# Optimization experiments

Measured on AMD Instinct MI355X. Metric: run time of the kernel, lower is better.

Reference implementation:

```python
import jax, jax.numpy as jnp
import numpy as np

N_SLOTS, KEY_DIM, VAL_DIM = 8192, 64, 64
B, S, TOPK = 8, 2048, 8


def setup_inputs() -> dict:
    key = jax.random.key(0)
    k1, k2, k3, k4, k5 = jax.random.split(key, 5)
    queries = jax.random.normal(k1, (B, S, KEY_DIM), dtype=jnp.float32)
    keys_mem = jax.random.normal(k2, (N_SLOTS, KEY_DIM), dtype=jnp.float32) * 0.02
    vals_mem = jax.random.normal(k3, (N_SLOTS, VAL_DIM), dtype=jnp.float32) * 0.02
    fast_vals = jax.random.normal(k4, (N_SLOTS, VAL_DIM), dtype=jnp.float32) * 0.01
    timestamps = jax.random.uniform(k5, (N_SLOTS,), dtype=jnp.float32)
    return {
        "queries": queries,
        "keys_mem": keys_mem,
        "vals_mem": vals_mem,
        "fast_vals": fast_vals,
        "timestamps": timestamps,
        "topk": TOPK,
    }


def reference(queries, keys_mem, vals_mem, fast_vals, timestamps, topk):
    # sim: [B, S, n_slots], scaled dot-product vs. memory keys
    scale = keys_mem.shape[1] ** (-0.5)
    sim = jnp.einsum("bsd,nd->bsn", queries, keys_mem) * scale
    # topk indices computed on detached scores (torch uses sim.detach())
    _, idx = jax.lax.top_k(jax.lax.stop_gradient(sim), topk)  # idx: [B, S, k]
    # gather topk similarities (torch does this via one-hot * sim; same math)
    sim_topk = jnp.take_along_axis(sim, idx, axis=-1)  # [B, S, k]
    # effective memory = slow + fast store; gather rows (torch: one_hot @ memory)
    effective_memory = vals_mem + fast_vals  # [n_slots, val_dim]
    gathered_vals = effective_memory[idx]  # [B, S, k, val_dim]
    attn_weights = jax.nn.softmax(sim_topk, axis=-1)  # [B, S, k]
    weighted_vals = gathered_vals * attn_weights[..., None]  # [B, S, k, val_dim]
    ts_retrieved = timestamps[idx]  # [B, S, k]
    return weighted_vals, idx, ts_retrieved
```

## Files before the change

### kernel.cpp

```cpp
#include <hip/hip_runtime.h>
#include <math.h>

#define NQ      16384
#define NSLOTS  8192
#define D       64
#define K       8

#define WV_ELEMS  (NQ * K * D)
#define IDX_OFF   (WV_ELEMS)
#define TSO_OFF   (IDX_OFF + NQ * K)

#define QPB    32
#define BLOCK  512
#define WAVES  8
#define SPW    (NSLOTS / WAVES)
#define ITERS  (SPW / 32)

using short8  = __attribute__((ext_vector_type(8))) short;
using bf16x8  = __attribute__((ext_vector_type(8))) __bf16;
using f32x4   = __attribute__((ext_vector_type(4))) float;

#define MFMA_BF16(A, B, C) __builtin_amdgcn_mfma_f32_16x16x32_bf16((A), (B), (C), 0, 0, 0)

__device__ __forceinline__ bf16x8 load_frag(const unsigned short* p) {
    short8 s = *reinterpret_cast<const short8*>(p);
    return __builtin_bit_cast(bf16x8, s);
}

__device__ __forceinline__ float packkey(float s, int code) {
    unsigned u = __float_as_uint(s) & 0xFFFFE000u;
    return __uint_as_float(u | (unsigned)code);
}

__device__ __forceinline__ void ins8(float (&tv)[8], float key) {
    float k2 = fmaxf(key, tv[0]);
    float o0 = fminf(tv[1], k2);
    float o1 = __builtin_amdgcn_fmed3f(tv[1], tv[2], k2);
    float o2 = __builtin_amdgcn_fmed3f(tv[2], tv[3], k2);
    float o3 = __builtin_amdgcn_fmed3f(tv[3], tv[4], k2);
    float o4 = __builtin_amdgcn_fmed3f(tv[4], tv[5], k2);
    float o5 = __builtin_amdgcn_fmed3f(tv[5], tv[6], k2);
    float o6 = __builtin_amdgcn_fmed3f(tv[6], tv[7], k2);
    float o7 = fmaxf(tv[7], k2);
    tv[0]=o0; tv[1]=o1; tv[2]=o2; tv[3]=o3; tv[4]=o4; tv[5]=o5; tv[6]=o6; tv[7]=o7;
}

__device__ __forceinline__ void cs(float& a, float& b) {
    const float lo = fminf(a, b), hi = fmaxf(a, b);
    a = lo; b = hi;
}
__device__ __forceinline__ void sort_bitonic8(float (&v)[8]) {
    cs(v[0],v[4]); cs(v[1],v[5]); cs(v[2],v[6]); cs(v[3],v[7]);
    cs(v[0],v[2]); cs(v[1],v[3]); cs(v[4],v[6]); cs(v[5],v[7]);
    cs(v[0],v[1]); cs(v[2],v[3]); cs(v[4],v[5]); cs(v[6],v[7]);
}

__device__ __forceinline__ unsigned short f2bf(float f) {
    unsigned u = __float_as_uint(f);
    return (unsigned short)((u + 0x7FFFu + ((u >> 16) & 1u)) >> 16);
}

__global__ __launch_bounds__(256)
void conv_kernel(const float* __restrict__ q, const float* __restrict__ k,
                 unsigned short* __restrict__ ws) {
    const int t = blockIdx.x * blockDim.x + threadIdx.x;
    if (t < 262144) {
        float4 v = reinterpret_cast<const float4*>(q)[t];
        unsigned long long r =
              (unsigned long long)f2bf(v.x * 0.125f)
            | ((unsigned long long)f2bf(v.y * 0.125f) << 16)
            | ((unsigned long long)f2bf(v.z * 0.125f) << 32)
            | ((unsigned long long)f2bf(v.w * 0.125f) << 48);
        reinterpret_cast<unsigned long long*>(ws + 524288)[t] = r;
    } else if (t < 393216) {
        const int i = t - 262144;
        float4 v = reinterpret_cast<const float4*>(k)[i];
        unsigned long long r =
              (unsigned long long)f2bf(v.x)
            | ((unsigned long long)f2bf(v.y) << 16)
            | ((unsigned long long)f2bf(v.z) << 32)
            | ((unsigned long long)f2bf(v.w) << 48);
        reinterpret_cast<unsigned long long*>(ws)[i] = r;
    }
}

__global__ __launch_bounds__(BLOCK, 4)
void ltm_mfma_kernel(const float* __restrict__ queries,
                     const float* __restrict__ keys_mem,
                     const float* __restrict__ vals_mem,
                     const float* __restrict__ fast_vals,
                     const float* __restrict__ timestamps,
                     const unsigned short* __restrict__ kb,
                     const unsigned short* __restrict__ qb,
                     float* __restrict__ out)
{
    __shared__ float candk[QPB][68];

    const int tid  = threadIdx.x;
    const int lane = tid & 63;
    const int w    = tid >> 6;
    const int row  = lane & 15;
    const int g    = lane >> 4;
    const int g4   = g * 4;
    const int koff = g * 8;
    const int qbase = blockIdx.x * QPB;

    const unsigned short* qpA = qb + (size_t)(qbase + row) * D + koff;
    const bf16x8 bA0 = load_frag(qpA);
    const bf16x8 bA1 = load_frag(qpA + 32);
    const bf16x8 bB0 = load_frag(qpA + 16 * D);
    const bf16x8 bB1 = load_frag(qpA + 16 * D + 32);

    float tvA[8], tvB[8];
    #pragma unroll
    for (int i = 0; i < 8; ++i) { tvA[i] = -INFINITY; tvB[i] = -INFINITY; }

    const int wbase = w * SPW;
    const unsigned short* kp0 = kb + (size_t)(wbase + row) * D + koff;
    bf16x8 a00 = load_frag(kp0);
    bf16x8 a01 = load_frag(kp0 + 32);
    bf16x8 a10 = load_frag(kp0 + 16 * D);
    bf16x8 a11 = load_frag(kp0 + 16 * D + 32);

    int codeA = 8191 - (wbase + g4);

    #pragma unroll 2
    for (int it = 0; it < ITERS; ++it) {
        const int snext = wbase + (it + 1) * 32;
        const unsigned short* np_ = kb + (size_t)(snext + row) * D + koff;
        bf16x8 n00 = load_frag(np_);
        bf16x8 n01 = load_frag(np_ + 32);
        bf16x8 n10 = load_frag(np_ + 16 * D);
        bf16x8 n11 = load_frag(np_ + 16 * D + 32);

        const f32x4 z = {0.f, 0.f, 0.f, 0.f};
        f32x4 c00 = MFMA_BF16(a00, bA0, z);  c00 = MFMA_BF16(a01, bA1, c00);
        f32x4 c01 = MFMA_BF16(a00, bB0, z);  c01 = MFMA_BF16(a01, bB1, c01);
        f32x4 c10 = MFMA_BF16(a10, bA0, z);  c10 = MFMA_BF16(a11, bA1, c10);
        f32x4 c11 = MFMA_BF16(a10, bB0, z);  c11 = MFMA_BF16(a11, bB1, c11);

        ins8(tvA, packkey(c00[0], codeA     ));
        ins8(tvA, packkey(c00[1], codeA -  1));
        ins8(tvA, packkey(c00[2], codeA -  2));
        ins8(tvA, packkey(c00[3], codeA -  3));
        ins8(tvA, packkey(c10[0], codeA - 16));
        ins8(tvA, packkey(c10[1], codeA - 17));
        ins8(tvA, packkey(c10[2], codeA - 18));
        ins8(tvA, packkey(c10[3], codeA - 19));
        ins8(tvB, packkey(c01[0], codeA     ));
        ins8(tvB, packkey(c01[1], codeA -  1));
        ins8(tvB, packkey(c01[2], codeA -  2));
        ins8(tvB, packkey(c01[3], codeA -  3));
        ins8(tvB, packkey(c11[0], codeA - 16));
        ins8(tvB, packkey(c11[1], codeA - 17));
        ins8(tvB, packkey(c11[2], codeA - 18));
        ins8(tvB, packkey(c11[3], codeA - 19));

        codeA -= 32;
        a00 = n00; a01 = n01; a10 = n10; a11 = n11;
    }

    {
        float sA[8], sB[8];
        #pragma unroll
        for (int j = 0; j < 8; ++j) {
            sA[j] = __shfl_xor(tvA[j], 32, 64);
            sB[j] = __shfl_xor(tvB[j], 32, 64);
        }
        float mA[8], mB[8];
        #pragma unroll
        for (int j = 0; j < 8; ++j) {
            mA[j] = fmaxf(tvA[j], sA[7 - j]);
            mB[j] = fmaxf(tvB[j], sB[7 - j]);
        }
        sort_bitonic8(mA);
        sort_bitonic8(mB);
        #pragma unroll
        for (int j = 0; j < 8; ++j) {
            sA[j] = __shfl_xor(mA[j], 16, 64);
            sB[j] = __shfl_xor(mB[j], 16, 64);
        }
        if (g == 0) {
            #pragma unroll
            for (int j = 0; j < 8; ++j) {
                candk[row     ][w * 8 + j] = fmaxf(mA[j], sA[7 - j]);
                candk[row + 16][w * 8 + j] = fmaxf(mB[j], sB[7 - j]);
            }
        }
    }
    __syncthreads();

    const int ql = tid >> 4;
    const int ls = tid & 15;
    const int q  = qbase + ql;

    const float4 qc = reinterpret_cast<const float4*>(queries)[q * 16 + ls];

    unsigned long long tk[8];
    #pragma unroll
    for (int i = 0; i < 8; ++i) tk[i] = 0ull;

    for (int j = 0; j < 64; ++j) {
        const float fk  = candk[ql][j];
        const int   sid = 8191 - (int)(__float_as_uint(fk) & 8191u);
        const float4 kc = reinterpret_cast<const float4*>(keys_mem)[sid * 16 + ls];
        float p = qc.x * kc.x;
        p = fmaf(qc.y, kc.y, p);
        p = fmaf(qc.z, kc.z, p);
        p = fmaf(qc.w, kc.w, p);
        p += __shfl_xor(p, 1, 64);
        p += __shfl_xor(p, 2, 64);
        p += __shfl_xor(p, 4, 64);
        p += __shfl_xor(p, 8, 64);
        const float s = p * 0.125f;
        const unsigned u  = __float_as_uint(s);
        const unsigned ou = (u & 0x80000000u) ? ~u : (u | 0x80000000u);
        const unsigned long long key =
            ((unsigned long long)ou << 13) | (unsigned)(8191 - sid);
        if (key > tk[0]) {
            tk[0] = key;
            #pragma unroll
            for (int uu = 0; uu < 7; ++uu) {
                const bool sw = tk[uu] > tk[uu + 1];
                const unsigned long long x = sw ? tk[uu + 1] : tk[uu];
                const unsigned long long y = sw ? tk[uu]     : tk[uu + 1];
                tk[uu] = x; tk[uu + 1] = y;
            }
        }
    }

    float wv[K]; int wi[K];
    #pragma unroll
    for (int r = 0; r < K; ++r) {
        const unsigned long long best = tk[7 - r];
        const int      sid = 8191 - (int)(best & 8191ull);
        const unsigned ou  = (unsigned)(best >> 13);
        const unsigned ub  = (ou & 0x80000000u) ? (ou & 0x7FFFFFFFu) : ~ou;
        wv[r] = __uint_as_float(ub);
        wi[r] = sid;
    }
    const float m = wv[0];
    float e[K]; float sum = 0.f;
    #pragma unroll
    for (int r = 0; r < K; ++r) { e[r] = expf(wv[r] - m); sum += e[r]; }
    const float inv = 1.f / sum;

    {
        const int   r   = ls >> 1;
        const int   h   = ls & 1;
        const int   id  = wi[r];
        const float wgt = e[r] * inv;
        const float4* vp = reinterpret_cast<const float4*>(vals_mem)  + (size_t)id * 16 + h * 8;
        const float4* fp = reinterpret_cast<const float4*>(fast_vals) + (size_t)id * 16 + h * 8;
        float4* op = reinterpret_cast<float4*>(out + ((size_t)(q * K + r)) * D + h * 32);
        #pragma unroll
        for (int i = 0; i < 8; ++i) {
            const float4 a = vp[i];
            const float4 b = fp[i];
            float4 c;
            c.x = (a.x + b.x) * wgt;
            c.y = (a.y + b.y) * wgt;
            c.z = (a.z + b.z) * wgt;
            c.w = (a.w + b.w) * wgt;
            op[i] = c;
        }
        if (ls < 8) {
            out[IDX_OFF + (size_t)q * K + ls] = (float)wi[ls];
        } else {
            const int r2 = ls - 8;
            out[TSO_OFF + (size_t)q * K + r2] = timestamps[wi[r2]];
        }
    }
}

#define FQPB   32
#define FTPQ   8
#define FBLOCK 256
#define FTS    128
#define FLDK   68
#define FNTILES (NSLOTS / FTS)

__global__ __launch_bounds__(FBLOCK, 2)
void ltm_fused_kernel(const float* __restrict__ queries,
                      const float* __restrict__ keys_mem,
                      const float* __restrict__ vals_mem,
                      const float* __restrict__ fast_vals,
                      const float* __restrict__ timestamps,
                      float* __restrict__ out)
{
    __shared__ float kt[FTS * FLDK];
    __shared__ float candv[FQPB][FTPQ * K];
    __shared__ int   candi[FQPB][FTPQ * K];
    __shared__ float selw[FQPB][K];
    __shared__ int   seli[FQPB][K];

    const int tid = threadIdx.x;
    const int ql  = tid / FTPQ;
    const int sub = tid % FTPQ;
    const int q   = blockIdx.x * FQPB + ql;

    float4 qv[D / 4];
    {
        const float4* qp = reinterpret_cast<const float4*>(queries + (size_t)q * D);
        #pragma unroll
        for (int i = 0; i < D / 4; ++i) qv[i] = qp[i];
    }

    float tv[K]; int ti[K];
    #pragma unroll
    for (int i = 0; i < K; ++i) { tv[i] = -INFINITY; ti[i] = 0; }

    for (int tile = 0; tile < FNTILES; ++tile) {
        __syncthreads();
        {
            const float4* kg = reinterpret_cast<const float4*>(keys_mem + (size_t)tile * FTS * D);
            #pragma unroll
            for (int i = 0; i < (FTS * D / 4) / FBLOCK; ++i) {
                const int e = tid + i * FBLOCK;
                const int row = e >> 4;
                const int col = e & 15;
                *reinterpret_cast<float4*>(&kt[row * FLDK + col * 4]) = kg[e];
            }
        }
        __syncthreads();

        #pragma unroll 4
        for (int j = 0; j < FTS / FTPQ; ++j) {
            const int local = sub + j * FTPQ;
            const float* kr = &kt[local * FLDK];
            float4 a0 = make_float4(0.f, 0.f, 0.f, 0.f);
            float4 a1 = make_float4(0.f, 0.f, 0.f, 0.f);
            #pragma unroll
            for (int i = 0; i < D / 4; i += 2) {
                const float4 k0 = *reinterpret_cast<const float4*>(&kr[(i + 0) * 4]);
                const float4 k1 = *reinterpret_cast<const float4*>(&kr[(i + 1) * 4]);
                a0.x = fmaf(k0.x, qv[i].x, a0.x);   a0.y = fmaf(k0.y, qv[i].y, a0.y);
                a0.z = fmaf(k0.z, qv[i].z, a0.z);   a0.w = fmaf(k0.w, qv[i].w, a0.w);
                a1.x = fmaf(k1.x, qv[i+1].x, a1.x); a1.y = fmaf(k1.y, qv[i+1].y, a1.y);
                a1.z = fmaf(k1.z, qv[i+1].z, a1.z); a1.w = fmaf(k1.w, qv[i+1].w, a1.w);
            }
            float s = ((a0.x + a1.x) + (a0.y + a1.y)) + ((a0.z + a1.z) + (a0.w + a1.w));
            s *= 0.125f;
            const int gid = tile * FTS + local;
            if (s > tv[0]) {
                tv[0] = s; ti[0] = gid;
                #pragma unroll
                for (int u = 0; u < K - 1; ++u) {
                    const bool sw = tv[u] > tv[u + 1];
                    const float va = sw ? tv[u + 1] : tv[u];
                    const float vb = sw ? tv[u]     : tv[u + 1];
                    const int   ia = sw ? ti[u + 1] : ti[u];
                    const int   ib = sw ? ti[u]     : ti[u + 1];
                    tv[u] = va; tv[u + 1] = vb; ti[u] = ia; ti[u + 1] = ib;
                }
            }
        }
    }

    #pragma unroll
    for (int i = 0; i < K; ++i) {
        candv[ql][sub * K + i] = tv[i];
        candi[ql][sub * K + i] = ti[i];
    }
    __syncthreads();

    if (sub == 0) {
        float wv[K]; int wi[K];
        #pragma unroll
        for (int r = 0; r < K; ++r) {
            float bv = -INFINITY; int bi = 0x7fffffff; int bp = 0;
            for (int c = 0; c < FTPQ * K; ++c) {
                const float v = candv[ql][c];
                const int  id = candi[ql][c];
                if ((v > bv) || (v == bv && id < bi)) { bv = v; bi = id; bp = c; }
            }
            candv[ql][bp] = -INFINITY;
            wv[r] = bv; wi[r] = bi;
        }
        const float m = wv[0];
        float e[K]; float sum = 0.f;
        #pragma unroll
        for (int r = 0; r < K; ++r) { e[r] = expf(wv[r] - m); sum += e[r]; }
        const float inv = 1.f / sum;
        #pragma unroll
        for (int r = 0; r < K; ++r) { selw[ql][r] = e[r] * inv; seli[ql][r] = wi[r]; }
    }
    __syncthreads();

    {
        const int r = sub;
        const int id = seli[ql][r];
        const float w = selw[ql][r];
        const float4* vp = reinterpret_cast<const float4*>(vals_mem  + (size_t)id * D);
        const float4* fp = reinterpret_cast<const float4*>(fast_vals + (size_t)id * D);
        float4* op = reinterpret_cast<float4*>(out + (size_t)(q * K + r) * D);
        #pragma unroll
        for (int i = 0; i < D / 4; ++i) {
            const float4 a = vp[i];
            const float4 b = fp[i];
            float4 c;
            c.x = (a.x + b.x) * w; c.y = (a.y + b.y) * w;
            c.z = (a.z + b.z) * w; c.w = (a.w + b.w) * w;
            op[i] = c;
        }
        out[IDX_OFF + (size_t)q * K + r] = (float)id;
        out[TSO_OFF + (size_t)q * K + r] = timestamps[id];
    }
}

extern "C" void kernel_launch(void* const* d_in, const int* in_sizes, int n_in,
                              void* d_out, int out_size, void* d_ws, size_t ws_size,
                              hipStream_t stream) {
    (void)in_sizes; (void)n_in; (void)out_size;
    const float* queries    = (const float*)d_in[0];
    const float* keys_mem   = (const float*)d_in[1];
    const float* vals_mem   = (const float*)d_in[2];
    const float* fast_vals  = (const float*)d_in[3];
    const float* timestamps = (const float*)d_in[4];
    float* out = (float*)d_out;

    if (ws_size >= (size_t)3 * 1024 * 1024) {
        unsigned short* ws = (unsigned short*)d_ws;
        conv_kernel<<<1536, 256, 0, stream>>>(queries, keys_mem, ws);
        ltm_mfma_kernel<<<NQ / QPB, BLOCK, 0, stream>>>(
            queries, keys_mem, vals_mem, fast_vals, timestamps,
            ws , ws + 524288 , out);
    } else {
        ltm_fused_kernel<<<NQ / FQPB, FBLOCK, 0, stream>>>(
            queries, keys_mem, vals_mem, fast_vals, timestamps, out);
    }
}
```

Measured before the change: 126.9 us.

## Halve queries per block to 16 and remap refine/output phase to 32 lanes per query

Cuts queries per block from 32 to 16, so each wave computes only one 16-query MFMA column group and keeps one top-8 list instead of two. Occupancy hints rise to 8 blocks per CU and the grid doubles. The fp32 re-scoring and output phase now uses 32 lanes per query with float2 loads and an extra shuffle step. Per-block register pressure drops, but each key fragment loaded is reused across half as many queries, doubling key traffic and MFMA issue per useful score.

```diff
diff --git a/kernel.cpp b/kernel.cpp
--- a/kernel.cpp
+++ b/kernel.cpp
@@ -10,7 +10,7 @@
 #define IDX_OFF   (WV_ELEMS)
 #define TSO_OFF   (IDX_OFF + NQ * K)
 
-#define QPB    32
+#define QPB    16
 #define BLOCK  512
 #define WAVES  8
 #define SPW    (NSLOTS / WAVES)
@@ -84,7 +84,7 @@
     }
 }
 
-__global__ __launch_bounds__(BLOCK, 4)
+__global__ __launch_bounds__(BLOCK, 8)
 void ltm_mfma_kernel(const float* __restrict__ queries,
                      const float* __restrict__ keys_mem,
                      const float* __restrict__ vals_mem,
@@ -108,12 +108,10 @@
     const unsigned short* qpA = qb + (size_t)(qbase + row) * D + koff;
     const bf16x8 bA0 = load_frag(qpA);
     const bf16x8 bA1 = load_frag(qpA + 32);
-    const bf16x8 bB0 = load_frag(qpA + 16 * D);
-    const bf16x8 bB1 = load_frag(qpA + 16 * D + 32);
-
-    float tvA[8], tvB[8];
-    #pragma unroll
-    for (int i = 0; i < 8; ++i) { tvA[i] = -INFINITY; tvB[i] = -INFINITY; }
+
+    float tvA[8];
+    #pragma unroll
+    for (int i = 0; i < 8; ++i) tvA[i] = -INFINITY;
 
     const int wbase = w * SPW;
     const unsigned short* kp0 = kb + (size_t)(wbase + row) * D + koff;
@@ -134,84 +132,62 @@
         bf16x8 n11 = load_frag(np_ + 16 * D + 32);
 
         const f32x4 z = {0.f, 0.f, 0.f, 0.f};
-        f32x4 c00 = MFMA_BF16(a00, bA0, z);  c00 = MFMA_BF16(a01, bA1, c00);
-        f32x4 c01 = MFMA_BF16(a00, bB0, z);  c01 = MFMA_BF16(a01, bB1, c01);
-        f32x4 c10 = MFMA_BF16(a10, bA0, z);  c10 = MFMA_BF16(a11, bA1, c10);
-        f32x4 c11 = MFMA_BF16(a10, bB0, z);  c11 = MFMA_BF16(a11, bB1, c11);
-
-        ins8(tvA, packkey(c00[0], codeA     ));
-        ins8(tvA, packkey(c00[1], codeA -  1));
-        ins8(tvA, packkey(c00[2], codeA -  2));
-        ins8(tvA, packkey(c00[3], codeA -  3));
-        ins8(tvA, packkey(c10[0], codeA - 16));
-        ins8(tvA, packkey(c10[1], codeA - 17));
-        ins8(tvA, packkey(c10[2], codeA - 18));
-        ins8(tvA, packkey(c10[3], codeA - 19));
-        ins8(tvB, packkey(c01[0], codeA     ));
-        ins8(tvB, packkey(c01[1], codeA -  1));
-        ins8(tvB, packkey(c01[2], codeA -  2));
-        ins8(tvB, packkey(c01[3], codeA -  3));
-        ins8(tvB, packkey(c11[0], codeA - 16));
-        ins8(tvB, packkey(c11[1], codeA - 17));
-        ins8(tvB, packkey(c11[2], codeA - 18));
-        ins8(tvB, packkey(c11[3], codeA - 19));
+        f32x4 c0 = MFMA_BF16(a00, bA0, z);  c0 = MFMA_BF16(a01, bA1, c0);
+        f32x4 c1 = MFMA_BF16(a10, bA0, z);  c1 = MFMA_BF16(a11, bA1, c1);
+
+        ins8(tvA, packkey(c0[0], codeA     ));
+        ins8(tvA, packkey(c0[1], codeA -  1));
+        ins8(tvA, packkey(c0[2], codeA -  2));
+        ins8(tvA, packkey(c0[3], codeA -  3));
+        ins8(tvA, packkey(c1[0], codeA - 16));
+        ins8(tvA, packkey(c1[1], codeA - 17));
+        ins8(tvA, packkey(c1[2], codeA - 18));
+        ins8(tvA, packkey(c1[3], codeA - 19));
 
         codeA -= 32;
         a00 = n00; a01 = n01; a10 = n10; a11 = n11;
     }
 
     {
-        float sA[8], sB[8];
-        #pragma unroll
-        for (int j = 0; j < 8; ++j) {
-            sA[j] = __shfl_xor(tvA[j], 32, 64);
-            sB[j] = __shfl_xor(tvB[j], 32, 64);
-        }
-        float mA[8], mB[8];
-        #pragma unroll
-        for (int j = 0; j < 8; ++j) {
-            mA[j] = fmaxf(tvA[j], sA[7 - j]);
-            mB[j] = fmaxf(tvB[j], sB[7 - j]);
-        }
+        float sA[8];
+        #pragma unroll
+        for (int j = 0; j < 8; ++j) sA[j] = __shfl_xor(tvA[j], 32, 64);
+        float mA[8];
+        #pragma unroll
+        for (int j = 0; j < 8; ++j) mA[j] = fmaxf(tvA[j], sA[7 - j]);
         sort_bitonic8(mA);
-        sort_bitonic8(mB);
-        #pragma unroll
-        for (int j = 0; j < 8; ++j) {
-            sA[j] = __shfl_xor(mA[j], 16, 64);
-            sB[j] = __shfl_xor(mB[j], 16, 64);
-        }
+        #pragma unroll
+        for (int j = 0; j < 8; ++j) sA[j] = __shfl_xor(mA[j], 16, 64);
         if (g == 0) {
             #pragma unroll
-            for (int j = 0; j < 8; ++j) {
-                candk[row     ][w * 8 + j] = fmaxf(mA[j], sA[7 - j]);
-                candk[row + 16][w * 8 + j] = fmaxf(mB[j], sB[7 - j]);
-            }
+            for (int j = 0; j < 8; ++j)
+                candk[row][w * 8 + j] = fmaxf(mA[j], sA[7 - j]);
         }
     }
     __syncthreads();
 
-    const int ql = tid >> 4;
-    const int ls = tid & 15;
-    const int q  = qbase + ql;
-
-    const float4 qc = reinterpret_cast<const float4*>(queries)[q * 16 + ls];
+    const int h  = lane >> 5;
+    const int ls = lane & 31;
+    const int qi = 2 * w + h;
+    const int q  = qbase + qi;
+
+    const float2 qc = reinterpret_cast<const float2*>(queries)[q * 32 + ls];
 
     unsigned long long tk[8];
     #pragma unroll
     for (int i = 0; i < 8; ++i) tk[i] = 0ull;
 
     for (int j = 0; j < 64; ++j) {
-        const float fk  = candk[ql][j];
+        const float fk  = candk[qi][j];
         const int   sid = 8191 - (int)(__float_as_uint(fk) & 8191u);
-        const float4 kc = reinterpret_cast<const float4*>(keys_mem)[sid * 16 + ls];
+        const float2 kc = reinterpret_cast<const float2*>(keys_mem)[sid * 32 + ls];
         float p = qc.x * kc.x;
         p = fmaf(qc.y, kc.y, p);
-        p = fmaf(qc.z, kc.z, p);
-        p = fmaf(qc.w, kc.w, p);
         p += __shfl_xor(p, 1, 64);
         p += __shfl_xor(p, 2, 64);
         p += __shfl_xor(p, 4, 64);
         p += __shfl_xor(p, 8, 64);
+        p += __shfl_xor(p, 16, 64);
         const float s = p * 0.125f;
         const unsigned u  = __float_as_uint(s);
         const unsigned ou = (u & 0x80000000u) ? ~u : (u | 0x80000000u);
@@ -246,15 +222,15 @@
     const float inv = 1.f / sum;
 
     {
-        const int   r   = ls >> 1;
-        const int   h   = ls & 1;
+        const int   r   = ls >> 2;
+        const int   s4  = ls & 3;
         const int   id  = wi[r];
         const float wgt = e[r] * inv;
-        const float4* vp = reinterpret_cast<const float4*>(vals_mem)  + (size_t)id * 16 + h * 8;
-        const float4* fp = reinterpret_cast<const float4*>(fast_vals) + (size_t)id * 16 + h * 8;
-        float4* op = reinterpret_cast<float4*>(out + ((size_t)(q * K + r)) * D + h * 32);
-        #pragma unroll
-        for (int i = 0; i < 8; ++i) {
+        const float4* vp = reinterpret_cast<const float4*>(vals_mem)  + (size_t)id * 16 + s4 * 4;
+        const float4* fp = reinterpret_cast<const float4*>(fast_vals) + (size_t)id * 16 + s4 * 4;
+        float4* op = reinterpret_cast<float4*>(out) + ((size_t)(q * K + r)) * 16 + s4 * 4;
+        #pragma unroll
+        for (int i = 0; i < 4; ++i) {
             const float4 a = vp[i];
             const float4 b = fp[i];
             float4 c;
@@ -266,7 +242,7 @@
         }
         if (ls < 8) {
             out[IDX_OFF + (size_t)q * K + ls] = (float)wi[ls];
-        } else {
+        } else if (ls < 16) {
             const int r2 = ls - 8;
             out[TSO_OFF + (size_t)q * K + r2] = timestamps[wi[r2]];
         }
```

After: 176.6 us. +39.2%, slower.

## Split candidate rescoring across 4 subgroups per query with shuffle top-k merge

Applied to the files above, without the earlier changes.

The exact fp32 rescoring of the 64 candidates per query previously used all 16 lanes per candidate, one candidate at a time, with a 4-step shuffle reduction. Now the 16 lanes form 4 subgroups of 4 lanes. Each subgroup rescores 16 candidates with 16-float dot products and a 2-step reduction, and keeps its own top-8. The subgroup lists are then merged with two rounds of 64-bit shuffles and bitonic sorts. This cuts the serial loop length and shuffle count, at the cost of extra registers and a merge stage.

```diff
diff --git a/kernel.cpp b/kernel.cpp
--- a/kernel.cpp
+++ b/kernel.cpp
@@ -53,6 +53,18 @@
     cs(v[0],v[4]); cs(v[1],v[5]); cs(v[2],v[6]); cs(v[3],v[7]);
     cs(v[0],v[2]); cs(v[1],v[3]); cs(v[4],v[6]); cs(v[5],v[7]);
     cs(v[0],v[1]); cs(v[2],v[3]); cs(v[4],v[5]); cs(v[6],v[7]);
+}
+
+__device__ __forceinline__ void csu(unsigned long long& a, unsigned long long& b) {
+    const bool lt = a < b;
+    const unsigned long long lo = lt ? a : b;
+    const unsigned long long hi = lt ? b : a;
+    a = lo; b = hi;
+}
+__device__ __forceinline__ void sort_bitonic8_u64(unsigned long long (&v)[8]) {
+    csu(v[0],v[4]); csu(v[1],v[5]); csu(v[2],v[6]); csu(v[3],v[7]);
+    csu(v[0],v[2]); csu(v[1],v[3]); csu(v[4],v[6]); csu(v[5],v[7]);
+    csu(v[0],v[1]); csu(v[2],v[3]); csu(v[4],v[5]); csu(v[6],v[7]);
 }
 
 __device__ __forceinline__ unsigned short f2bf(float f) {
@@ -190,28 +202,39 @@
     }
     __syncthreads();
 
-    const int ql = tid >> 4;
-    const int ls = tid & 15;
-    const int q  = qbase + ql;
-
-    const float4 qc = reinterpret_cast<const float4*>(queries)[q * 16 + ls];
+    const int ql  = tid >> 4;
+    const int l16 = tid & 15;
+    const int sg  = l16 >> 2;
+    const int ls4 = l16 & 3;
+    const int q   = qbase + ql;
+
+    float4 qv4[4];
+    {
+        const float4* qp = reinterpret_cast<const float4*>(queries) + (size_t)q * 16 + ls4 * 4;
+        #pragma unroll
+        for (int i = 0; i < 4; ++i) qv4[i] = qp[i];
+    }
 
     unsigned long long tk[8];
     #pragma unroll
     for (int i = 0; i < 8; ++i) tk[i] = 0ull;
 
-    for (int j = 0; j < 64; ++j) {
-        const float fk  = candk[ql][j];
+    #pragma unroll 4
+    for (int jt = 0; jt < 16; ++jt) {
+        const float fk  = candk[ql][sg * 16 + jt];
         const int   sid = 8191 - (int)(__float_as_uint(fk) & 8191u);
-        const float4 kc = reinterpret_cast<const float4*>(keys_mem)[sid * 16 + ls];
-        float p = qc.x * kc.x;
-        p = fmaf(qc.y, kc.y, p);
-        p = fmaf(qc.z, kc.z, p);
-        p = fmaf(qc.w, kc.w, p);
+        const float4* kp = reinterpret_cast<const float4*>(keys_mem) + (size_t)sid * 16 + ls4 * 4;
+        float p = 0.f;
+        #pragma unroll
+        for (int i = 0; i < 4; ++i) {
+            const float4 kc = kp[i];
+            p = fmaf(qv4[i].x, kc.x, p);
+            p = fmaf(qv4[i].y, kc.y, p);
+            p = fmaf(qv4[i].z, kc.z, p);
+            p = fmaf(qv4[i].w, kc.w, p);
+        }
         p += __shfl_xor(p, 1, 64);
         p += __shfl_xor(p, 2, 64);
-        p += __shfl_xor(p, 4, 64);
-        p += __shfl_xor(p, 8, 64);
         const float s = p * 0.125f;
         const unsigned u  = __float_as_uint(s);
         const unsigned ou = (u & 0x80000000u) ? ~u : (u | 0x80000000u);
@@ -229,6 +252,21 @@
         }
     }
 
+    #pragma unroll
+    for (int st = 4; st <= 8; st <<= 1) {
+        unsigned long long sk[8], mk[8];
+        #pragma unroll
+        for (int j = 0; j < 8; ++j) sk[j] = __shfl_xor(tk[j], st, 64);
+        #pragma unroll
+        for (int j = 0; j < 8; ++j) {
+            const unsigned long long a = tk[j], b = sk[7 - j];
+            mk[j] = a > b ? a : b;
+        }
+        sort_bitonic8_u64(mk);
+        #pragma unroll
+        for (int j = 0; j < 8; ++j) tk[j] = mk[j];
+    }
+
     float wv[K]; int wi[K];
     #pragma unroll
     for (int r = 0; r < K; ++r) {
@@ -246,13 +284,13 @@
     const float inv = 1.f / sum;
 
     {
-        const int   r   = ls >> 1;
-        const int   h   = ls & 1;
+        const int   r   = l16 >> 1;
+        const int   h   = l16 & 1;
         const int   id  = wi[r];
         const float wgt = e[r] * inv;
         const float4* vp = reinterpret_cast<const float4*>(vals_mem)  + (size_t)id * 16 + h * 8;
         const float4* fp = reinterpret_cast<const float4*>(fast_vals) + (size_t)id * 16 + h * 8;
-        float4* op = reinterpret_cast<float4*>(out + ((size_t)(q * K + r)) * D + h * 32);
+        float4* op = reinterpret_cast<float4*>(out) + ((size_t)(q * K + r)) * 16 + h * 8;
         #pragma unroll
         for (int i = 0; i < 8; ++i) {
             const float4 a = vp[i];
@@ -264,10 +302,10 @@
             c.w = (a.w + b.w) * wgt;
             op[i] = c;
         }
-        if (ls < 8) {
-            out[IDX_OFF + (size_t)q * K + ls] = (float)wi[ls];
+        if (l16 < 8) {
+            out[IDX_OFF + (size_t)q * K + l16] = (float)wi[l16];
         } else {
-            const int r2 = ls - 8;
+            const int r2 = l16 - 8;
             out[TSO_OFF + (size_t)q * K + r2] = timestamps[wi[r2]];
         }
     }
```

Result: faster. 109.5 us (-13.7%).
